# Optimization experiments

Measured on AMD Instinct MI355X. Metric: run time of the kernel, lower is better.

Reference implementation:

```python
import jax, jax.numpy as jnp
import numpy as np

# NSA hyperparams (match init_kwargs)
D_BLK = 64    # d: block stride
L_CMP = 64    # compression block length (== d -> non-overlapping blocks)
L_SLC = 64    # selection block length (== l_cmp == d -> P_slc = P_cmp)
BQ = 64       # block_size_q
TOPK = 16     # slc_top_k
WL, WR = 512, 0  # sliding window (left, right)


def _nsa_forward(q, k, v, w_k, b_k, w_v, b_v, w_gate, b_gate, seqlen):
    S, qh, dim = q.shape
    kv = k.shape[1]
    H = qh // kv
    b = S // seqlen          # number of equal-length packed sequences
    s = seqlen
    scale = dim ** -0.5
    f32 = jnp.float32

    # [b, s, kv, H, e]: q head g*H+h belongs to kv head g (repeat_interleave layout)
    q5 = q.reshape(b, s, kv, H, dim)
    k3 = k.reshape(b, s, kv, dim)
    v3 = v.reshape(b, s, kv, dim)

    # ---- block compression (extract_blocks + cmp_linear over block length) ----
    n_blk = s // D_BLK
    kb = k.reshape(b, n_blk, D_BLK, kv, dim)
    vb = v.reshape(b, n_blk, D_BLK, kv, dim)
    K_cmp = jnp.einsum('bntke,t->bnke', kb, w_k) + b_k[0]
    V_cmp = jnp.einsum('bntke,t->bnke', vb, w_v) + b_v[0]

    # ---- compressed attention (per sequence, fp32 softmax) ----
    sc = jnp.einsum('bqkhe,bnke->bkhqn', q5, K_cmp).astype(f32) * scale
    P = jax.nn.softmax(sc, axis=-1)
    out_cmp = jnp.einsum('bkhqn,bnke->bqkhe', P.astype(q.dtype), V_cmp)

    # ---- selection scores: pool P over q-blocks and GQA groups, then top-k ----
    nqb = s // BQ
    pooled = P.reshape(b, kv, H, nqb, BQ, n_blk).sum(axis=(2, 4))  # [b,kv,nqb,n_blk]
    idx = jax.lax.top_k(pooled, TOPK)[1]                            # [b,kv,nqb,TOPK]

    # gather selected K/V blocks (shared by all queries in a q-block / GQA group)
    kb2 = jnp.transpose(kb, (0, 3, 1, 2, 4))  # [b,kv,n_blk,l,e]
    vb2 = jnp.transpose(vb, (0, 3, 1, 2, 4))
    gather = jax.vmap(jax.vmap(lambda blocks, i: blocks[i]))
    K_sel = gather(kb2, idx)  # [b,kv,nqb,TOPK,l,e]
    V_sel = gather(vb2, idx)

    # ---- selected-block attention ----
    qblk = q5.reshape(b, nqb, BQ, kv, H, dim)
    sc2 = jnp.einsum('bnckhe,bkntle->bkhnctl', qblk, K_sel).astype(f32) * scale
    sc2 = sc2.reshape(b, kv, H, nqb, BQ, TOPK * L_SLC)
    P2 = jax.nn.softmax(sc2, axis=-1).astype(q.dtype)
    out_slc = jnp.einsum('bkhncm,bknme->bnckhe', P2,
                         V_sel.reshape(b, kv, nqb, TOPK * L_SLC, dim))
    out_slc = out_slc.reshape(b, s, kv, H, dim)

    # ---- sliding-window attention (window_size=(WL, WR), non-causal flag) ----
    sw = jnp.einsum('bikhe,bjke->bkhij', q5, k3).astype(f32) * scale
    i = jnp.arange(s)[:, None]
    j = jnp.arange(s)[None, :]
    valid = (j >= i - WL) & (j <= i + WR)
    sw = jnp.where(valid, sw, -jnp.inf)
    Pw = jax.nn.softmax(sw, axis=-1).astype(q.dtype)
    out_win = jnp.einsum('bkhij,bjke->bikhe', Pw, v3)

    # ---- gated fusion of the three branches ----
    gate = jax.nn.sigmoid(jnp.einsum('bqkhe,ec->bqkhc', q5, w_gate) + b_gate)
    out = (gate[..., 0:1] * out_cmp
           + gate[..., 1:2] * out_slc
           + gate[..., 2:3] * out_win)
    return out.reshape(S, qh, dim)


def setup_inputs() -> dict:
    key = jax.random.key(0)
    ks = jax.random.split(key, 9)
    S, qh, kvh, dim = 4096, 8, 2, 128
    inp = {
        'q': jax.random.normal(ks[0], (S, qh, dim), jnp.float32),
        'k': jax.random.normal(ks[1], (S, kvh, dim), jnp.float32),
        'v': jax.random.normal(ks[2], (S, kvh, dim), jnp.float32),
        'w_k': jax.random.normal(ks[3], (L_CMP,), jnp.float32) * (L_CMP ** -0.5),
        'b_k': jax.random.normal(ks[4], (1,), jnp.float32) * 0.02,
        'w_v': jax.random.normal(ks[5], (L_CMP,), jnp.float32) * (L_CMP ** -0.5),
        'b_v': jax.random.normal(ks[6], (1,), jnp.float32) * 0.02,
        'w_gate': jax.random.normal(ks[7], (dim, 3), jnp.float32) * (dim ** -0.5),
        'b_gate': jax.random.normal(ks[8], (3,), jnp.float32) * 0.02,
        'seqlen': 2048,
    }
    return inp


def reference(q, k, v, w_k, b_k, w_v, b_v, w_gate, b_gate, seqlen):
    return _nsa_forward(q, k, v, w_k, b_k, w_v, b_v, w_gate, b_gate, seqlen)
```

## Files before the change

kernel.cpp:

```cpp
#include <hip/hip_runtime.h>
#include <hip/hip_bf16.h>


#define SEQ   2048
#define NB    2
#define KV    2
#define NH    4
#define QH    8
#define DIM   128
#define NBLK  32
#define NQB   32
#define NTOP  16
#define SCALE 0.08838834764831845f
#define QSC   0.12751831795244785f
#define VP    72
#define VCS   40

typedef unsigned short ushort_t;
using bf16x8 = __attribute__((ext_vector_type(8))) short;
using f32x4  = __attribute__((ext_vector_type(4))) float;

__device__ __forceinline__ unsigned pkbf(float a, float b){
  union { __hip_bfloat162 h; unsigned u; } cv;
  cv.h = __float22bfloat162_rn(make_float2(a, b));
  return cv.u;
}
__device__ __forceinline__ ushort_t b16(float f){
  union { float f; unsigned i; } x; x.f = f;
  unsigned r = x.i + 0x7fffu + ((x.i >> 16) & 1u);
  return (ushort_t)(r >> 16);
}
__device__ __forceinline__ float fb(ushort_t h){
  union { unsigned i; float f; } x; x.i = ((unsigned)h) << 16;
  return x.f;
}

__device__ __forceinline__ void async16(ushort_t* l, const ushort_t* g){
  __builtin_amdgcn_global_load_lds(
      (const __attribute__((address_space(1))) unsigned int*)(size_t)g,
      (__attribute__((address_space(3))) unsigned int*)(size_t)l,
      16, 0, 0);
}

__global__ __launch_bounds__(256) void prep_k(
    const float* __restrict__ k, const float* __restrict__ v,
    const float* __restrict__ w_k, const float* __restrict__ b_k,
    const float* __restrict__ w_v, const float* __restrict__ b_v,
    ushort_t* __restrict__ Kb, ushort_t* __restrict__ VT,
    float* __restrict__ Kc, float* __restrict__ Vc)
{
  int blk = blockIdx.x;
  int db = blk & 1, rb = (blk >> 1) & 31, bbg = blk >> 6;
  int bb = bbg >> 1, g = bbg & 1;
  int tid = threadIdx.x;
  __shared__ ushort_t T[64*VP];
  __shared__ float wks[64], wvs[64];
  __shared__ float accK[16][64], accV[16][64];

  if (tid < 64){ wks[tid] = w_k[tid]; wvs[tid] = w_v[tid]; }
  __syncthreads();

  float4 sk = {0,0,0,0}, sv = {0,0,0,0};
  for (int jj = 0; jj < 4; ++jj){
    int i = tid + jj*256;
    int r = i >> 4, ds = i & 15;
    size_t src = ((size_t)(bb*SEQ + rb*64 + r)*KV + g)*DIM + db*64 + ds*4;
    float4 kx = *(const float4*)(k + src);
    float4 vx = *(const float4*)(v + src);
    uint2 kk; kk.x = pkbf(kx.x,kx.y); kk.y = pkbf(kx.z,kx.w);
    size_t rowb = ((size_t)bbg*SEQ + rb*64 + r)*DIM*2;
    int swz = (db*128 + ds*8) ^ ((r & 7) << 4);
    *(uint2*)((char*)Kb + rowb + swz) = kk;
    unsigned v01 = pkbf(vx.x,vx.y), v23 = pkbf(vx.z,vx.w);
    T[(ds*4+0)*VP + r] = (ushort_t)(v01 & 0xffffu);
    T[(ds*4+1)*VP + r] = (ushort_t)(v01 >> 16);
    T[(ds*4+2)*VP + r] = (ushort_t)(v23 & 0xffffu);
    T[(ds*4+3)*VP + r] = (ushort_t)(v23 >> 16);
    float a = wks[r], b = wvs[r];
    sk.x += a*kx.x; sk.y += a*kx.y; sk.z += a*kx.z; sk.w += a*kx.w;
    sv.x += b*vx.x; sv.y += b*vx.y; sv.z += b*vx.z; sv.w += b*vx.w;
  }
  *(float4*)&accK[tid>>4][(tid&15)*4] = sk;
  *(float4*)&accV[tid>>4][(tid&15)*4] = sv;
  __syncthreads();

  for (int jj = 0; jj < 4; ++jj){
    int i = tid + jj*256;
    int d = i >> 4, seg = i & 15;
    uint2 u = *(uint2*)&T[d*VP + seg*4];
    size_t rowb = ((size_t)bbg*DIM + db*64 + d)*SEQ*2;
    int swz = (seg*8) ^ ((d & 7) << 4);
    *(uint2*)((char*)VT + rowb + rb*128 + swz) = u;
  }

  size_t obase = ((size_t)(bbg*NBLK + rb))*DIM + db*64;
  if (tid < 64){
    float s = 0.f;
#pragma unroll
    for (int i = 0; i < 16; ++i) s += accK[i][tid];
    Kc[obase + tid] = s + b_k[0];
  } else if (tid < 128){
    int d = tid - 64;
    float s = 0.f;
#pragma unroll
    for (int i = 0; i < 16; ++i) s += accV[i][d];
    Vc[obase + d] = s + b_v[0];
  }
}

__global__ __launch_bounds__(512, 2) void attn_k(
    const float* __restrict__ q, const ushort_t* __restrict__ Kb,
    const ushort_t* __restrict__ VT,
    const float* __restrict__ Kc, const float* __restrict__ Vc,
    const float* __restrict__ w_gate, const float* __restrict__ b_gate,
    float* __restrict__ slcbuf, float* __restrict__ out)
{
  int idx = blockIdx.x;
  int x = idx & 7, low = idx & 1, u = idx >> 3;
  int bbg = x >> 1;
  int j = u*2 + low;
  int role = j >> 5;
  int qb = j & 31;
  int bb = bbg >> 1, g = bbg & 1;

  int tid = threadIdx.x;
  int lane = tid & 63, w = tid >> 6;
  int quad = lane >> 4, l15 = lane & 15;
  int h = w & 3, qh2 = w >> 2;
  int xr = (l15 & 7) << 4;

  __shared__ ushort_t Ks[2][64*128];
  __shared__ ushort_t VTs[2][128*64];
  __shared__ ushort_t Ps[256*VP];
  __shared__ ushort_t VcTh[128*VCS];
  __shared__ ushort_t VcTl[128*VCS];
  __shared__ float pw[8][NBLK];
  __shared__ float gbuf[256];
  __shared__ int   idxs[NTOP];

  if (role == 0){
    {
      int key = tid >> 4, dq = tid & 15;
      const float* kcs = Kc + ((size_t)bbg*NBLK + key)*DIM + dq*8;
      float4 f0 = *(const float4*)kcs, f1 = *(const float4*)(kcs + 4);
      float fe[8] = {f0.x,f0.y,f0.z,f0.w,f1.x,f1.y,f1.z,f1.w};
      union { ushort_t u[8]; uint4 v; } hi, lo;
#pragma unroll
      for (int e = 0; e < 8; ++e){
        ushort_t hh = b16(fe[e]);
        hi.u[e] = hh; lo.u[e] = b16(fe[e] - fb(hh));
      }
      int off = (dq*16) ^ ((key & 7) << 4);
      *(uint4*)((char*)&Ks[0][0] + key*256 + off) = hi.v;
      *(uint4*)((char*)&Ks[0][0] + (key+32)*256 + off) = lo.v;
    }
    {
      int d = tid & 127, kq = tid >> 7;
      const float* vcs = Vc + (size_t)bbg*NBLK*DIM + d;
      union { ushort_t u[8]; uint4 v; } hi, lo;
#pragma unroll
      for (int kk = 0; kk < 8; ++kk){
        float f = vcs[(kq*8 + kk)*DIM];
        ushort_t hh = b16(f);
        hi.u[kk] = hh; lo.u[kk] = b16(f - fb(hh));
      }
      *(uint4*)&VcTh[d*VCS + kq*8] = hi.v;
      *(uint4*)&VcTl[d*VCS + kq*8] = lo.v;
    }
  }

  const float* qrow0 = q + ((size_t)(bb*SEQ + qb*64 + qh2*32 + l15)*QH + g*NH + h)*DIM;
  const float* qrow1 = qrow0 + (size_t)16*QH*DIM;
  int gcol = 1 + role;
  bf16x8 qfrag0[4], qfrag1[4], qlo0[4], qlo1[4];
  float gp0 = 0.f, gp1 = 0.f, gc0 = 0.f, gc1 = 0.f;
#pragma unroll
  for (int kc = 0; kc < 4; ++kc){
    int d0 = kc*32 + quad*8;
    float4 a0 = *(const float4*)(qrow0 + d0);
    float4 a1 = *(const float4*)(qrow0 + d0 + 4);
    float4 b0 = *(const float4*)(qrow1 + d0);
    float4 b1 = *(const float4*)(qrow1 + d0 + 4);
    float qa[8] = {a0.x,a0.y,a0.z,a0.w,a1.x,a1.y,a1.z,a1.w};
    float qc[8] = {b0.x,b0.y,b0.z,b0.w,b1.x,b1.y,b1.z,b1.w};
#pragma unroll
    for (int jj = 0; jj < 8; ++jj){
      float wg = w_gate[(d0+jj)*3 + gcol];
      gp0 += qa[jj]*wg; gp1 += qc[jj]*wg;
    }
    if (role == 0){
#pragma unroll
      for (int jj = 0; jj < 8; ++jj){
        float w0 = w_gate[(d0+jj)*3];
        gc0 += qa[jj]*w0; gc1 += qc[jj]*w0;
      }
      union { ushort_t u[8]; bf16x8 v; } h0, l0, h1, l1;
#pragma unroll
      for (int e = 0; e < 8; ++e){
        float s0f = qa[e]*QSC; ushort_t hh0 = b16(s0f);
        h0.u[e] = hh0; l0.u[e] = b16(s0f - fb(hh0));
        float s1f = qc[e]*QSC; ushort_t hh1 = b16(s1f);
        h1.u[e] = hh1; l1.u[e] = b16(s1f - fb(hh1));
      }
      qfrag0[kc] = h0.v; qlo0[kc] = l0.v;
      qfrag1[kc] = h1.v; qlo1[kc] = l1.v;
    } else {
      union { unsigned uu[4]; bf16x8 v8; } t0, t1;
#pragma unroll
      for (int p2 = 0; p2 < 4; ++p2){
        t0.uu[p2] = pkbf(qa[2*p2]*QSC, qa[2*p2+1]*QSC);
        t1.uu[p2] = pkbf(qc[2*p2]*QSC, qc[2*p2+1]*QSC);
      }
      qfrag0[kc] = t0.v8; qfrag1[kc] = t1.v8;
    }
  }
  gp0 += __shfl_xor(gp0,16); gp0 += __shfl_xor(gp0,32);
  gp1 += __shfl_xor(gp1,16); gp1 += __shfl_xor(gp1,32);
  if (quad == 0){
    gbuf[w*32 + l15]      = 1.f/(1.f + __expf(-(gp0 + b_gate[gcol])));
    gbuf[w*32 + 16 + l15] = 1.f/(1.f + __expf(-(gp1 + b_gate[gcol])));
  }
  float g0c0 = 0.f, g0c1 = 0.f;
  if (role == 0){
    gc0 += __shfl_xor(gc0,16); gc0 += __shfl_xor(gc0,32);
    gc1 += __shfl_xor(gc1,16); gc1 += __shfl_xor(gc1,32);
    g0c0 = 1.f/(1.f + __expf(-(gc0 + b_gate[0])));
    g0c1 = 1.f/(1.f + __expf(-(gc1 + b_gate[0])));
  }
  __syncthreads();
  float gl0[4], gl1[4];
#pragma unroll
  for (int r = 0; r < 4; ++r){
    gl0[r] = gbuf[w*32 + quad*4 + r];
    gl1[r] = gbuf[w*32 + 16 + quad*4 + r];
  }

  const f32x4 zero4 = {0.f,0.f,0.f,0.f};
  f32x4 cp0[2], cp1[2];
  cp0[0] = zero4; cp0[1] = zero4; cp1[0] = zero4; cp1[1] = zero4;

  if (role == 0){
    f32x4 c0[2], c1[2];
    c0[0]=zero4; c0[1]=zero4; c1[0]=zero4; c1[1]=zero4;
#pragma unroll
    for (int kc = 0; kc < 4; ++kc){
#pragma unroll
      for (int nt = 0; nt < 2; ++nt){
        bf16x8 ah = *(bf16x8*)((char*)&Ks[0][0] + (nt*16 + l15)*256
                               + ((kc*64 + quad*16) ^ xr));
        bf16x8 al = *(bf16x8*)((char*)&Ks[0][0] + (nt*16 + l15 + 32)*256
                               + ((kc*64 + quad*16) ^ xr));
        c0[nt] = __builtin_amdgcn_mfma_f32_16x16x32_bf16(ah, qfrag0[kc], c0[nt], 0, 0, 0);
        c0[nt] = __builtin_amdgcn_mfma_f32_16x16x32_bf16(ah, qlo0[kc],   c0[nt], 0, 0, 0);
        c0[nt] = __builtin_amdgcn_mfma_f32_16x16x32_bf16(al, qfrag0[kc], c0[nt], 0, 0, 0);
        c1[nt] = __builtin_amdgcn_mfma_f32_16x16x32_bf16(ah, qfrag1[kc], c1[nt], 0, 0, 0);
        c1[nt] = __builtin_amdgcn_mfma_f32_16x16x32_bf16(ah, qlo1[kc],   c1[nt], 0, 0, 0);
        c1[nt] = __builtin_amdgcn_mfma_f32_16x16x32_bf16(al, qfrag1[kc], c1[nt], 0, 0, 0);
      }
    }
    float mx0 = -INFINITY, mx1 = -INFINITY;
#pragma unroll
    for (int nt = 0; nt < 2; ++nt)
#pragma unroll
      for (int r = 0; r < 4; ++r){
        mx0 = fmaxf(mx0, c0[nt][r]); mx1 = fmaxf(mx1, c1[nt][r]);
      }
    mx0 = fmaxf(mx0, __shfl_xor(mx0,16)); mx0 = fmaxf(mx0, __shfl_xor(mx0,32));
    mx1 = fmaxf(mx1, __shfl_xor(mx1,16)); mx1 = fmaxf(mx1, __shfl_xor(mx1,32));
    float s0 = 0.f, s1 = 0.f;
#pragma unroll
    for (int nt = 0; nt < 2; ++nt)
#pragma unroll
      for (int r = 0; r < 4; ++r){
        float p0v = exp2f(c0[nt][r] - mx0); c0[nt][r] = p0v; s0 += p0v;
        float p1v = exp2f(c1[nt][r] - mx1); c1[nt][r] = p1v; s1 += p1v;
      }
    s0 += __shfl_xor(s0,16); s0 += __shfl_xor(s0,32);
    s1 += __shfl_xor(s1,16); s1 += __shfl_xor(s1,32);
    float ip0 = 1.f/s0, ip1 = 1.f/s1;
    float ig0 = g0c0*ip0, ig1 = g0c1*ip1;
#pragma unroll
    for (int nt = 0; nt < 2; ++nt)
#pragma unroll
      for (int r = 0; r < 4; ++r){
        cp0[nt][r] = c0[nt][r]*ig0;
        cp1[nt][r] = c1[nt][r]*ig1;
        float t = c0[nt][r]*ip0 + c1[nt][r]*ip1;
        t += __shfl_xor(t,1); t += __shfl_xor(t,2);
        t += __shfl_xor(t,4); t += __shfl_xor(t,8);
        if (l15 == 0) pw[w][nt*16 + quad*4 + r] = t;
      }
    __syncthreads();
    if (tid < 64){
      int n = lane;
      float val = -INFINITY;
      if (n < NBLK){
        float sm = 0.f;
#pragma unroll
        for (int w2 = 0; w2 < 8; ++w2) sm += pw[w2][n];
        val = sm;
      }
      for (int t = 0; t < NTOP; ++t){
        float bv = val; int bi = n;
        for (int mm = 1; mm < 32; mm <<= 1){
          float ov = __shfl_xor(bv, mm);
          int   oi = __shfl_xor(bi, mm);
          if (ov > bv || (ov == bv && oi < bi)){ bv = ov; bi = oi; }
        }
        if (lane == 0) idxs[t] = bi;
        if (n == bi) val = -INFINITY;
      }
    }
    __syncthreads();
  }

  const ushort_t* kbase  = Kb + (size_t)bbg*SEQ*DIM;
  const ushort_t* vtbase = VT + (size_t)bbg*DIM*SEQ;

  int kb0 = (qb >= 8) ? (qb - 8) : 0;
  int nph = (role == 0) ? NTOP : (qb - kb0 + 1);
  int qi0 = qh2*32 + l15, qi1 = qi0 + 16;

  float m10 = -INFINITY, l10 = 0.f, m11 = -INFINITY, l11 = 0.f;
  f32x4 oacc0[8], oacc1[8];
#pragma unroll
  for (int dt = 0; dt < 8; ++dt){ oacc0[dt] = zero4; oacc1[dt] = zero4; }

  auto stage = [&](int bufi, int kb_){
    const ushort_t* ksrc = kbase + (size_t)kb_*64*DIM;
#pragma unroll
    for (int jj = 0; jj < 2; ++jj)
      async16(&Ks[bufi][(jj*512 + w*64)*8], ksrc + (size_t)(tid + jj*512)*8);
    const ushort_t* vsrc = vtbase + kb_*64;
#pragma unroll
    for (int jj = 0; jj < 2; ++jj){
      int i = tid + jj*512;
      int d = i >> 3, sg = i & 7;
      async16(&VTs[bufi][(jj*512 + w*64)*8], vsrc + (size_t)d*SEQ + sg*8);
    }
  };

  stage(0, (role == 0) ? idxs[0] : kb0);

  for (int t = 0; t < nph; ++t){
    int cur = t & 1;
    int kb = (role == 0) ? idxs[t] : (kb0 + t);
    __syncthreads();
    if (t+1 < nph){
      int kbn = (role == 0) ? idxs[t+1] : (kb0 + t + 1);
      stage(cur ^ 1, kbn);
    }
    __builtin_amdgcn_sched_barrier(0);

    f32x4 sacc0[4], sacc1[4];
#pragma unroll
    for (int nt = 0; nt < 4; ++nt){ sacc0[nt] = zero4; sacc1[nt] = zero4; }
    __builtin_amdgcn_s_setprio(1);
#pragma unroll
    for (int kc = 0; kc < 4; ++kc){
#pragma unroll
      for (int nt = 0; nt < 4; ++nt){
        bf16x8 a = *(bf16x8*)((char*)&Ks[cur][0] + (nt*16 + l15)*256
                              + ((kc*64 + quad*16) ^ xr));
        sacc0[nt] = __builtin_amdgcn_mfma_f32_16x16x32_bf16(a, qfrag0[kc], sacc0[nt], 0, 0, 0);
        sacc1[nt] = __builtin_amdgcn_mfma_f32_16x16x32_bf16(a, qfrag1[kc], sacc1[nt], 0, 0, 0);
      }
    }
    __builtin_amdgcn_s_setprio(0);

    bool mlow  = (role == 1) && (kb == qb - 8);
    bool mhigh = (role == 1) && (kb == qb);
    bool domask = mlow | mhigh;

    auto softmax_qt = [&](f32x4* sc2, float& m1r, float& l1r, int qi_l,
                          bool& skipped) -> float {
      float mx = -INFINITY;
      if (domask){
#pragma unroll
        for (int nt = 0; nt < 4; ++nt)
#pragma unroll
          for (int r = 0; r < 4; ++r){
            int key = nt*16 + quad*4 + r;
            float sv = sc2[nt][r];
            bool valid = (!mlow || key >= qi_l) && (!mhigh || key <= qi_l);
            sv = valid ? sv : -INFINITY;
            sc2[nt][r] = sv;
            mx = fmaxf(mx, sv);
          }
      } else {
#pragma unroll
        for (int nt = 0; nt < 4; ++nt)
#pragma unroll
          for (int r = 0; r < 4; ++r) mx = fmaxf(mx, sc2[nt][r]);
      }
      mx = fmaxf(mx, __shfl_xor(mx, 16));
      mx = fmaxf(mx, __shfl_xor(mx, 32));
      float al = 1.f;
      skipped = __all(mx <= m1r + 8.f);
      if (!skipped){
        float mn = fmaxf(m1r, mx);
        al = exp2f(m1r - mn);
        m1r = mn;
      }
      float s0 = 0.f;
#pragma unroll
      for (int nt = 0; nt < 4; ++nt)
#pragma unroll
        for (int r = 0; r < 4; ++r){
          float pe = exp2f(sc2[nt][r] - m1r);
          sc2[nt][r] = pe;
          s0 += pe;
        }
      s0 += __shfl_xor(s0, 16);
      s0 += __shfl_xor(s0, 32);
      l1r = l1r*al + s0;
      return al;
    };
    bool sk0, sk1;
    float al0 = softmax_qt(sacc0, m10, l10, qi0, sk0);
    float al1 = softmax_qt(sacc1, m11, l11, qi1, sk1);

#pragma unroll
    for (int nt = 0; nt < 4; ++nt){
      uint2 p0, p1;
      p0.x = pkbf(sacc0[nt][0], sacc0[nt][1]);
      p0.y = pkbf(sacc0[nt][2], sacc0[nt][3]);
      p1.x = pkbf(sacc1[nt][0], sacc1[nt][1]);
      p1.y = pkbf(sacc1[nt][2], sacc1[nt][3]);
      *(uint2*)&Ps[(w*32 + l15)*VP + nt*16 + quad*4] = p0;
      *(uint2*)&Ps[(w*32 + 16 + l15)*VP + nt*16 + quad*4] = p1;
    }

    if (!sk0){
      float ar[4];
#pragma unroll
      for (int r = 0; r < 4; ++r) ar[r] = __shfl(al0, quad*4 + r);
#pragma unroll
      for (int dt = 0; dt < 8; ++dt)
#pragma unroll
        for (int r = 0; r < 4; ++r) oacc0[dt][r] *= ar[r];
    }
    if (!sk1){
      float ar[4];
#pragma unroll
      for (int r = 0; r < 4; ++r) ar[r] = __shfl(al1, quad*4 + r);
#pragma unroll
      for (int dt = 0; dt < 8; ++dt)
#pragma unroll
        for (int r = 0; r < 4; ++r) oacc1[dt][r] *= ar[r];
    }

#pragma unroll
    for (int kc2 = 0; kc2 < 2; ++kc2){
      bf16x8 pa0 = *(bf16x8*)&Ps[(w*32 + l15)*VP + kc2*32 + quad*8];
      bf16x8 pa1 = *(bf16x8*)&Ps[(w*32 + 16 + l15)*VP + kc2*32 + quad*8];
      __builtin_amdgcn_s_setprio(1);
#pragma unroll
      for (int dt = 0; dt < 8; ++dt){
        bf16x8 vb8 = *(bf16x8*)((char*)&VTs[cur][0] + (dt*16 + l15)*128
                                + ((kc2*64 + quad*16) ^ xr));
        oacc0[dt] = __builtin_amdgcn_mfma_f32_16x16x32_bf16(pa0, vb8, oacc0[dt], 0, 0, 0);
        oacc1[dt] = __builtin_amdgcn_mfma_f32_16x16x32_bf16(pa1, vb8, oacc1[dt], 0, 0, 0);
      }
      __builtin_amdgcn_s_setprio(0);
    }
  }

  float lr0[4], lr1[4];
#pragma unroll
  for (int r = 0; r < 4; ++r){
    lr0[r] = __shfl(l10, quad*4 + r);
    lr1[r] = __shfl(l11, quad*4 + r);
  }
  if (role == 0){
    float a0[4], a1[4];
#pragma unroll
    for (int r = 0; r < 4; ++r){ a0[r] = gl0[r]/lr0[r]; a1[r] = gl1[r]/lr1[r]; }
#pragma unroll
    for (int dt = 0; dt < 8; ++dt)
#pragma unroll
      for (int r = 0; r < 4; ++r){ oacc0[dt][r] *= a0[r]; oacc1[dt][r] *= a1[r]; }
#pragma unroll
    for (int nt = 0; nt < 2; ++nt){
      union { ushort_t u[4]; uint2 v; } h0, l0, h1, l1;
#pragma unroll
      for (int r = 0; r < 4; ++r){
        ushort_t hh0 = b16(cp0[nt][r]);
        h0.u[r] = hh0; l0.u[r] = b16(cp0[nt][r] - fb(hh0));
        ushort_t hh1 = b16(cp1[nt][r]);
        h1.u[r] = hh1; l1.u[r] = b16(cp1[nt][r] - fb(hh1));
      }
      *(uint2*)&Ps[(w*32 + l15)*VP + nt*16 + quad*4]      = h0.v;
      *(uint2*)&Ps[(w*32 + l15)*VP + 32 + nt*16 + quad*4] = l0.v;
      *(uint2*)&Ps[(w*32 + 16 + l15)*VP + nt*16 + quad*4]      = h1.v;
      *(uint2*)&Ps[(w*32 + 16 + l15)*VP + 32 + nt*16 + quad*4] = l1.v;
    }
    bf16x8 pah0 = *(bf16x8*)&Ps[(w*32 + l15)*VP + quad*8];
    bf16x8 pal0 = *(bf16x8*)&Ps[(w*32 + l15)*VP + 32 + quad*8];
    bf16x8 pah1 = *(bf16x8*)&Ps[(w*32 + 16 + l15)*VP + quad*8];
    bf16x8 pal1 = *(bf16x8*)&Ps[(w*32 + 16 + l15)*VP + 32 + quad*8];
#pragma unroll
    for (int dt = 0; dt < 8; ++dt){
      bf16x8 vbh = *(bf16x8*)&VcTh[(dt*16 + l15)*VCS + quad*8];
      bf16x8 vbl = *(bf16x8*)&VcTl[(dt*16 + l15)*VCS + quad*8];
      oacc0[dt] = __builtin_amdgcn_mfma_f32_16x16x32_bf16(pah0, vbh, oacc0[dt], 0, 0, 0);
      oacc0[dt] = __builtin_amdgcn_mfma_f32_16x16x32_bf16(pah0, vbl, oacc0[dt], 0, 0, 0);
      oacc0[dt] = __builtin_amdgcn_mfma_f32_16x16x32_bf16(pal0, vbh, oacc0[dt], 0, 0, 0);
      oacc1[dt] = __builtin_amdgcn_mfma_f32_16x16x32_bf16(pah1, vbh, oacc1[dt], 0, 0, 0);
      oacc1[dt] = __builtin_amdgcn_mfma_f32_16x16x32_bf16(pah1, vbl, oacc1[dt], 0, 0, 0);
      oacc1[dt] = __builtin_amdgcn_mfma_f32_16x16x32_bf16(pal1, vbh, oacc1[dt], 0, 0, 0);
    }
#pragma unroll
    for (int r = 0; r < 4; ++r){
      size_t ob0 = ((size_t)(bb*SEQ + qb*64 + qh2*32 + quad*4 + r)*QH + g*NH + h)*DIM + l15;
      size_t ob1 = ob0 + (size_t)16*QH*DIM;
      float* op0 = slcbuf + ob0;
      float* op1 = slcbuf + ob1;
#pragma unroll
      for (int dt = 0; dt < 8; ++dt){
        op0[dt*16] = oacc0[dt][r];
        op1[dt*16] = oacc1[dt][r];
      }
    }
  } else {
#pragma unroll
    for (int r = 0; r < 4; ++r){
      float s20 = gl0[r] / lr0[r];
      float s21 = gl1[r] / lr1[r];
      size_t ob0 = ((size_t)(bb*SEQ + qb*64 + qh2*32 + quad*4 + r)*QH + g*NH + h)*DIM + l15;
      size_t ob1 = ob0 + (size_t)16*QH*DIM;
      float* op0 = out + ob0;
      float* op1 = out + ob1;
#pragma unroll
      for (int dt = 0; dt < 8; ++dt){
        op0[dt*16] = s20 * oacc0[dt][r];
        op1[dt*16] = s21 * oacc1[dt][r];
      }
    }
  }
}

__global__ __launch_bounds__(256) void merge_k(const float* __restrict__ slcbuf,
                                               float* __restrict__ out){
  int i = blockIdx.x * 256 + threadIdx.x;
  float4 a = ((const float4*)slcbuf)[i];
  float4 b = ((float4*)out)[i];
  b.x += a.x; b.y += a.y; b.z += a.z; b.w += a.w;
  ((float4*)out)[i] = b;
}

extern "C" void kernel_launch(void* const* d_in, const int* in_sizes, int n_in,
                              void* d_out, int out_size, void* d_ws, size_t ws_size,
                              hipStream_t stream) {
  const float* q      = (const float*)d_in[0];
  const float* k      = (const float*)d_in[1];
  const float* v      = (const float*)d_in[2];
  const float* w_k    = (const float*)d_in[3];
  const float* b_k    = (const float*)d_in[4];
  const float* w_v    = (const float*)d_in[5];
  const float* b_v    = (const float*)d_in[6];
  const float* w_gate = (const float*)d_in[7];
  const float* b_gate = (const float*)d_in[8];
  float* out = (float*)d_out;

  float* ws     = (float*)d_ws;
  float* Kc     = ws;
  float* Vc     = ws + 16384;
  float* slcbuf = ws + 49152;
  ushort_t* Kb  = (ushort_t*)(ws + 4243456);
  ushort_t* VT  = Kb + 1048576;

  prep_k <<<256, 256, 0, stream>>>(k, v, w_k, b_k, w_v, b_v, Kb, VT, Kc, Vc);
  attn_k <<<256, 512, 0, stream>>>(q, Kb, VT, Kc, Vc, w_gate, b_gate, slcbuf, out);
  merge_k<<<4096, 256, 0, stream>>>(slcbuf, out);
}
```

Measured before the change: 166.3 us.

## Software-pipeline PV matmul one step behind QK and use bitonic top-k

The attention loop now runs the P·V MFMA for the previous key block after the QK MFMA of the current block, so the softmax of one step overlaps with matrix work of another. To support this, V tiles get a third LDS buffer rotated between prev/cur/next, and the final P·V step is drained after the loop. The iterative 16-round shuffle argmax top-k is replaced by one bitonic sort over the 32 pooled scores, and the max and sum reductions are rewritten as trees. The cost is more LDS use and extra live registers for the deferred rescale state, which could reduce occupancy.

```diff
diff --git a/kernel.cpp b/kernel.cpp
--- a/kernel.cpp
+++ b/kernel.cpp
@@ -130,7 +130,7 @@
   int xr = (l15 & 7) << 4;
 
   __shared__ ushort_t Ks[2][64*128];
-  __shared__ ushort_t VTs[2][128*64];
+  __shared__ ushort_t VTs[3][128*64];
   __shared__ ushort_t Ps[256*VP];
   __shared__ ushort_t VcTh[128*VCS];
   __shared__ ushort_t VcTl[128*VCS];
@@ -300,16 +300,19 @@
         for (int w2 = 0; w2 < 8; ++w2) sm += pw[w2][n];
         val = sm;
       }
-      for (int t = 0; t < NTOP; ++t){
-        float bv = val; int bi = n;
-        for (int mm = 1; mm < 32; mm <<= 1){
-          float ov = __shfl_xor(bv, mm);
-          int   oi = __shfl_xor(bi, mm);
-          if (ov > bv || (ov == bv && oi < bi)){ bv = ov; bi = oi; }
+      int idxv = n;
+      for (int kk = 2; kk <= 32; kk <<= 1){
+        for (int jj2 = kk >> 1; jj2 > 0; jj2 >>= 1){
+          float pv = __shfl_xor(val, jj2);
+          int   pi = __shfl_xor(idxv, jj2);
+          bool lower = (lane & jj2) == 0;
+          bool desc  = (lane & kk) == 0;
+          bool iwin  = (val > pv) || (val == pv && idxv < pi);
+          bool keep  = (lower == desc) ? iwin : !iwin;
+          if (!keep){ val = pv; idxv = pi; }
         }
-        if (lane == 0) idxs[t] = bi;
-        if (n == bi) val = -INFINITY;
-      }
+      }
+      if (lane < NTOP) idxs[lane] = idxv;
     }
     __syncthreads();
   }
@@ -326,29 +329,32 @@
 #pragma unroll
   for (int dt = 0; dt < 8; ++dt){ oacc0[dt] = zero4; oacc1[dt] = zero4; }
 
-  auto stage = [&](int bufi, int kb_){
+  auto stage = [&](int kbuf, int vbuf, int kb_){
     const ushort_t* ksrc = kbase + (size_t)kb_*64*DIM;
 #pragma unroll
     for (int jj = 0; jj < 2; ++jj)
-      async16(&Ks[bufi][(jj*512 + w*64)*8], ksrc + (size_t)(tid + jj*512)*8);
+      async16(&Ks[kbuf][(jj*512 + w*64)*8], ksrc + (size_t)(tid + jj*512)*8);
     const ushort_t* vsrc = vtbase + kb_*64;
 #pragma unroll
     for (int jj = 0; jj < 2; ++jj){
       int i = tid + jj*512;
       int d = i >> 3, sg = i & 7;
-      async16(&VTs[bufi][(jj*512 + w*64)*8], vsrc + (size_t)d*SEQ + sg*8);
+      async16(&VTs[vbuf][(jj*512 + w*64)*8], vsrc + (size_t)d*SEQ + sg*8);
     }
   };
 
-  stage(0, (role == 0) ? idxs[0] : kb0);
+  stage(0, 0, (role == 0) ? idxs[0] : kb0);
+
+  float alp0 = 1.f, alp1 = 1.f;
+  bool  skp0 = true,  skp1 = true;
+  int vprev = 2, vcur = 0, vnext = 1;
 
   for (int t = 0; t < nph; ++t){
-    int cur = t & 1;
     int kb = (role == 0) ? idxs[t] : (kb0 + t);
     __syncthreads();
     if (t+1 < nph){
       int kbn = (role == 0) ? idxs[t+1] : (kb0 + t + 1);
-      stage(cur ^ 1, kbn);
+      stage((t+1) & 1, vnext, kbn);
     }
     __builtin_amdgcn_sched_barrier(0);
 
@@ -360,7 +366,7 @@
     for (int kc = 0; kc < 4; ++kc){
 #pragma unroll
       for (int nt = 0; nt < 4; ++nt){
-        bf16x8 a = *(bf16x8*)((char*)&Ks[cur][0] + (nt*16 + l15)*256
+        bf16x8 a = *(bf16x8*)((char*)&Ks[t & 1][0] + (nt*16 + l15)*256
                               + ((kc*64 + quad*16) ^ xr));
         sacc0[nt] = __builtin_amdgcn_mfma_f32_16x16x32_bf16(a, qfrag0[kc], sacc0[nt], 0, 0, 0);
         sacc1[nt] = __builtin_amdgcn_mfma_f32_16x16x32_bf16(a, qfrag1[kc], sacc1[nt], 0, 0, 0);
@@ -368,31 +374,63 @@
     }
     __builtin_amdgcn_s_setprio(0);
 
+    if (t > 0){
+      if (!skp0){
+        float ar[4];
+#pragma unroll
+        for (int r = 0; r < 4; ++r) ar[r] = __shfl(alp0, quad*4 + r);
+#pragma unroll
+        for (int dt = 0; dt < 8; ++dt)
+#pragma unroll
+          for (int r = 0; r < 4; ++r) oacc0[dt][r] *= ar[r];
+      }
+      if (!skp1){
+        float ar[4];
+#pragma unroll
+        for (int r = 0; r < 4; ++r) ar[r] = __shfl(alp1, quad*4 + r);
+#pragma unroll
+        for (int dt = 0; dt < 8; ++dt)
+#pragma unroll
+          for (int r = 0; r < 4; ++r) oacc1[dt][r] *= ar[r];
+      }
+#pragma unroll
+      for (int kc2 = 0; kc2 < 2; ++kc2){
+        bf16x8 pa0 = *(bf16x8*)&Ps[(w*32 + l15)*VP + kc2*32 + quad*8];
+        bf16x8 pa1 = *(bf16x8*)&Ps[(w*32 + 16 + l15)*VP + kc2*32 + quad*8];
+        __builtin_amdgcn_s_setprio(1);
+#pragma unroll
+        for (int dt = 0; dt < 8; ++dt){
+          bf16x8 vb8 = *(bf16x8*)((char*)&VTs[vprev][0] + (dt*16 + l15)*128
+                                  + ((kc2*64 + quad*16) ^ xr));
+          oacc0[dt] = __builtin_amdgcn_mfma_f32_16x16x32_bf16(pa0, vb8, oacc0[dt], 0, 0, 0);
+          oacc1[dt] = __builtin_amdgcn_mfma_f32_16x16x32_bf16(pa1, vb8, oacc1[dt], 0, 0, 0);
+        }
+        __builtin_amdgcn_s_setprio(0);
+      }
+    }
+
     bool mlow  = (role == 1) && (kb == qb - 8);
     bool mhigh = (role == 1) && (kb == qb);
     bool domask = mlow | mhigh;
 
     auto softmax_qt = [&](f32x4* sc2, float& m1r, float& l1r, int qi_l,
                           bool& skipped) -> float {
-      float mx = -INFINITY;
       if (domask){
 #pragma unroll
         for (int nt = 0; nt < 4; ++nt)
 #pragma unroll
           for (int r = 0; r < 4; ++r){
             int key = nt*16 + quad*4 + r;
-            float sv = sc2[nt][r];
             bool valid = (!mlow || key >= qi_l) && (!mhigh || key <= qi_l);
-            sv = valid ? sv : -INFINITY;
-            sc2[nt][r] = sv;
-            mx = fmaxf(mx, sv);
+            sc2[nt][r] = valid ? sc2[nt][r] : -INFINITY;
           }
-      } else {
-#pragma unroll
-        for (int nt = 0; nt < 4; ++nt)
-#pragma unroll
-          for (int r = 0; r < 4; ++r) mx = fmaxf(mx, sc2[nt][r]);
-      }
+      }
+      float mnt[4];
+#pragma unroll
+      for (int nt = 0; nt < 4; ++nt)
+        mnt[nt] = fmaxf(fmaxf(sc2[nt][0], sc2[nt][1]),
+                        fmaxf(sc2[nt][2], sc2[nt][3]));
+      float mx = fmaxf(fmaxf(mnt[0], mnt[1]), fmaxf(mnt[2], mnt[3]));
       mx = fmaxf(mx, __shfl_xor(mx, 16));
       mx = fmaxf(mx, __shfl_xor(mx, 32));
       float al = 1.f;
@@ -402,15 +440,17 @@
         al = exp2f(m1r - mn);
         m1r = mn;
       }
-      float s0 = 0.f;
-#pragma unroll
-      for (int nt = 0; nt < 4; ++nt)
-#pragma unroll
-        for (int r = 0; r < 4; ++r){
-          float pe = exp2f(sc2[nt][r] - m1r);
-          sc2[nt][r] = pe;
-          s0 += pe;
-        }
+      float snt[4];
+#pragma unroll
+      for (int nt = 0; nt < 4; ++nt){
+        float p0 = exp2f(sc2[nt][0] - m1r);
+        float p1 = exp2f(sc2[nt][1] - m1r);
+        float p2 = exp2f(sc2[nt][2] - m1r);
+        float p3 = exp2f(sc2[nt][3] - m1r);
+        sc2[nt][0] = p0; sc2[nt][1] = p1; sc2[nt][2] = p2; sc2[nt][3] = p3;
+        snt[nt] = (p0 + p1) + (p2 + p3);
+      }
+      float s0 = (snt[0] + snt[1]) + (snt[2] + snt[3]);
       s0 += __shfl_xor(s0, 16);
       s0 += __shfl_xor(s0, 32);
       l1r = l1r*al + s0;
@@ -419,6 +459,8 @@
     bool sk0, sk1;
     float al0 = softmax_qt(sacc0, m10, l10, qi0, sk0);
     float al1 = softmax_qt(sacc1, m11, l11, qi1, sk1);
+    alp0 = al0; skp0 = sk0;
+    alp1 = al1; skp1 = sk1;
 
 #pragma unroll
     for (int nt = 0; nt < 4; ++nt){
@@ -431,38 +473,39 @@
       *(uint2*)&Ps[(w*32 + 16 + l15)*VP + nt*16 + quad*4] = p1;
     }
 
-    if (!sk0){
+    int tmpv = vprev; vprev = vcur; vcur = vnext; vnext = tmpv;
+  }
+
+  {
+    if (!skp0){
       float ar[4];
 #pragma unroll
-      for (int r = 0; r < 4; ++r) ar[r] = __shfl(al0, quad*4 + r);
+      for (int r = 0; r < 4; ++r) ar[r] = __shfl(alp0, quad*4 + r);
 #pragma unroll
       for (int dt = 0; dt < 8; ++dt)
 #pragma unroll
         for (int r = 0; r < 4; ++r) oacc0[dt][r] *= ar[r];
     }
-    if (!sk1){
+    if (!skp1){
       float ar[4];
 #pragma unroll
-      for (int r = 0; r < 4; ++r) ar[r] = __shfl(al1, quad*4 + r);
+      for (int r = 0; r < 4; ++r) ar[r] = __shfl(alp1, quad*4 + r);
 #pragma unroll
       for (int dt = 0; dt < 8; ++dt)
 #pragma unroll
         for (int r = 0; r < 4; ++r) oacc1[dt][r] *= ar[r];
     }
-
 #pragma unroll
     for (int kc2 = 0; kc2 < 2; ++kc2){
       bf16x8 pa0 = *(bf16x8*)&Ps[(w*32 + l15)*VP + kc2*32 + quad*8];
       bf16x8 pa1 = *(bf16x8*)&Ps[(w*32 + 16 + l15)*VP + kc2*32 + quad*8];
-      __builtin_amdgcn_s_setprio(1);
 #pragma unroll
       for (int dt = 0; dt < 8; ++dt){
-        bf16x8 vb8 = *(bf16x8*)((char*)&VTs[cur][0] + (dt*16 + l15)*128
+        bf16x8 vb8 = *(bf16x8*)((char*)&VTs[vprev][0] + (dt*16 + l15)*128
                                 + ((kc2*64 + quad*16) ^ xr));
         oacc0[dt] = __builtin_amdgcn_mfma_f32_16x16x32_bf16(pa0, vb8, oacc0[dt], 0, 0, 0);
         oacc1[dt] = __builtin_amdgcn_mfma_f32_16x16x32_bf16(pa1, vb8, oacc1[dt], 0, 0, 0);
       }
-      __builtin_amdgcn_s_setprio(0);
     }
   }
 
```

After: 162.9 us, median of 2. 2.1% less time.

## Process two KV blocks per iteration, read V from global, bitonic top-k

Applied to the files above, without the earlier changes.

Each attention iteration now handles two 64-key blocks (128 keys), which halves the number of phases and barriers. K is double-buffered in shared memory, while V^T is read directly from global memory into MFMA operands instead of being staged, and the V^T swizzle is dropped. The serial 16-round top-k arg-max is replaced with a wavefront bitonic sort. In exchange, register pressure rises from wider score tiles, V loads become unstaged global reads with possible latency stalls, and the window path adds an extra masked half-block.

```diff
diff --git a/kernel.cpp b/kernel.cpp
--- a/kernel.cpp
+++ b/kernel.cpp
@@ -14,6 +14,7 @@
 #define SCALE 0.08838834764831845f
 #define QSC   0.12751831795244785f
 #define VP    72
+#define PSP   136
 #define VCS   40
 
 typedef unsigned short ushort_t;
@@ -89,8 +90,7 @@
     int d = i >> 4, seg = i & 15;
     uint2 u = *(uint2*)&T[d*VP + seg*4];
     size_t rowb = ((size_t)bbg*DIM + db*64 + d)*SEQ*2;
-    int swz = (seg*8) ^ ((d & 7) << 4);
-    *(uint2*)((char*)VT + rowb + rb*128 + swz) = u;
+    *(uint2*)((char*)VT + rowb + rb*128 + seg*8) = u;
   }
 
   size_t obase = ((size_t)(bbg*NBLK + rb))*DIM + db*64;
@@ -129,9 +129,8 @@
   int h = w & 3, qh2 = w >> 2;
   int xr = (l15 & 7) << 4;
 
-  __shared__ ushort_t Ks[2][64*128];
-  __shared__ ushort_t VTs[2][128*64];
-  __shared__ ushort_t Ps[256*VP];
+  __shared__ ushort_t Ks[2][128*128];
+  __shared__ ushort_t Ps[256*PSP];
   __shared__ ushort_t VcTh[128*VCS];
   __shared__ ushort_t VcTl[128*VCS];
   __shared__ float pw[8][NBLK];
@@ -300,16 +299,19 @@
         for (int w2 = 0; w2 < 8; ++w2) sm += pw[w2][n];
         val = sm;
       }
-      for (int t = 0; t < NTOP; ++t){
-        float bv = val; int bi = n;
-        for (int mm = 1; mm < 32; mm <<= 1){
-          float ov = __shfl_xor(bv, mm);
-          int   oi = __shfl_xor(bi, mm);
-          if (ov > bv || (ov == bv && oi < bi)){ bv = ov; bi = oi; }
+      int idxv = n;
+      for (int kk = 2; kk <= 32; kk <<= 1){
+        for (int jj2 = kk >> 1; jj2 > 0; jj2 >>= 1){
+          float pv = __shfl_xor(val, jj2);
+          int   pi = __shfl_xor(idxv, jj2);
+          bool lower = (lane & jj2) == 0;
+          bool desc  = (lane & kk) == 0;
+          bool iwin  = (val > pv) || (val == pv && idxv < pi);
+          bool keep  = (lower == desc) ? iwin : !iwin;
+          if (!keep){ val = pv; idxv = pi; }
         }
-        if (lane == 0) idxs[t] = bi;
-        if (n == bi) val = -INFINITY;
-      }
+      }
+      if (lane < NTOP) idxs[lane] = idxv;
     }
     __syncthreads();
   }
@@ -318,48 +320,50 @@
   const ushort_t* vtbase = VT + (size_t)bbg*DIM*SEQ;
 
   int kb0 = (qb >= 8) ? (qb - 8) : 0;
-  int nph = (role == 0) ? NTOP : (qb - kb0 + 1);
+  int nph = (role == 0) ? 8 : ((qb < 8) ? ((qb >> 1) + 1) : 5);
   int qi0 = qh2*32 + l15, qi1 = qi0 + 16;
+  int hc0 = qb*64 + qi0 - kb0*64 - (nph - 1)*128;
+  int hc1 = hc0 + 16;
 
   float m10 = -INFINITY, l10 = 0.f, m11 = -INFINITY, l11 = 0.f;
   f32x4 oacc0[8], oacc1[8];
 #pragma unroll
   for (int dt = 0; dt < 8; ++dt){ oacc0[dt] = zero4; oacc1[dt] = zero4; }
 
-  auto stage = [&](int bufi, int kb_){
-    const ushort_t* ksrc = kbase + (size_t)kb_*64*DIM;
-#pragma unroll
-    for (int jj = 0; jj < 2; ++jj)
-      async16(&Ks[bufi][(jj*512 + w*64)*8], ksrc + (size_t)(tid + jj*512)*8);
-    const ushort_t* vsrc = vtbase + kb_*64;
-#pragma unroll
-    for (int jj = 0; jj < 2; ++jj){
-      int i = tid + jj*512;
-      int d = i >> 3, sg = i & 7;
-      async16(&VTs[bufi][(jj*512 + w*64)*8], vsrc + (size_t)d*SEQ + sg*8);
+  auto stageK = [&](int bufi, int rA, int rB){
+#pragma unroll
+    for (int jj = 0; jj < 4; ++jj){
+      int unit = tid + jj*512;
+      int row = unit >> 4, seg = unit & 15;
+      int absrow = (row < 64) ? (rA + row) : (rB + row - 64);
+      async16(&Ks[bufi][(jj*512 + w*64)*8],
+              kbase + (size_t)absrow*DIM + seg*8);
     }
   };
 
-  stage(0, (role == 0) ? idxs[0] : kb0);
+  if (role == 0) stageK(0, idxs[0]*64, idxs[1]*64);
+  else           stageK(0, kb0*64, kb0*64 + 64);
 
   for (int t = 0; t < nph; ++t){
     int cur = t & 1;
-    int kb = (role == 0) ? idxs[t] : (kb0 + t);
     __syncthreads();
     if (t+1 < nph){
-      int kbn = (role == 0) ? idxs[t+1] : (kb0 + t + 1);
-      stage(cur ^ 1, kbn);
+      if (role == 0) stageK(cur ^ 1, idxs[2*t+2]*64, idxs[2*t+3]*64);
+      else {
+        int rA = kb0*64 + (t+1)*128;
+        stageK(cur ^ 1, rA, rA + 64);
+      }
     }
     __builtin_amdgcn_sched_barrier(0);
 
-    f32x4 sacc0[4], sacc1[4];
-#pragma unroll
-    for (int nt = 0; nt < 4; ++nt){ sacc0[nt] = zero4; sacc1[nt] = zero4; }
+    f32x4 sacc0[8], sacc1[8];
+#pragma unroll
+    for (int nt = 0; nt < 8; ++nt){ sacc0[nt] = zero4; sacc1[nt] = zero4; }
     __builtin_amdgcn_s_setprio(1);
 #pragma unroll
     for (int kc = 0; kc < 4; ++kc){
 #pragma unroll
-      for (int nt = 0; nt < 4; ++nt){
+      for (int nt = 0; nt < 8; ++nt){
         bf16x8 a = *(bf16x8*)((char*)&Ks[cur][0] + (nt*16 + l15)*256
                               + ((kc*64 + quad*16) ^ xr));
         sacc0[nt] = __builtin_amdgcn_mfma_f32_16x16x32_bf16(a, qfrag0[kc], sacc0[nt], 0, 0, 0);
@@ -368,31 +372,29 @@
     }
     __builtin_amdgcn_s_setprio(0);
 
-    bool mlow  = (role == 1) && (kb == qb - 8);
-    bool mhigh = (role == 1) && (kb == qb);
-    bool domask = mlow | mhigh;
+    bool mlowP  = (role == 1) && (qb >= 8) && (t == 0);
+    bool mhighP = (role == 1) && (t == nph - 1);
+    bool domask = mlowP | mhighP;
 
     auto softmax_qt = [&](f32x4* sc2, float& m1r, float& l1r, int qi_l,
-                          bool& skipped) -> float {
-      float mx = -INFINITY;
+                          int hc_l, bool& skipped) -> float {
       if (domask){
 #pragma unroll
-        for (int nt = 0; nt < 4; ++nt)
+        for (int nt = 0; nt < 8; ++nt)
 #pragma unroll
           for (int r = 0; r < 4; ++r){
-            int key = nt*16 + quad*4 + r;
-            float sv = sc2[nt][r];
-            bool valid = (!mlow || key >= qi_l) && (!mhigh || key <= qi_l);
-            sv = valid ? sv : -INFINITY;
-            sc2[nt][r] = sv;
-            mx = fmaxf(mx, sv);
+            int kl = nt*16 + quad*4 + r;
+            bool valid = (!mlowP || kl >= qi_l) && (!mhighP || kl <= hc_l);
+            sc2[nt][r] = valid ? sc2[nt][r] : -INFINITY;
           }
-      } else {
-#pragma unroll
-        for (int nt = 0; nt < 4; ++nt)
-#pragma unroll
-          for (int r = 0; r < 4; ++r) mx = fmaxf(mx, sc2[nt][r]);
-      }
+      }
+      float mnt[8];
+#pragma unroll
+      for (int nt = 0; nt < 8; ++nt)
+        mnt[nt] = fmaxf(fmaxf(sc2[nt][0], sc2[nt][1]),
+                        fmaxf(sc2[nt][2], sc2[nt][3]));
+      float mx = fmaxf(fmaxf(fmaxf(mnt[0], mnt[1]), fmaxf(mnt[2], mnt[3])),
+                       fmaxf(fmaxf(mnt[4], mnt[5]), fmaxf(mnt[6], mnt[7])));
       mx = fmaxf(mx, __shfl_xor(mx, 16));
       mx = fmaxf(mx, __shfl_xor(mx, 32));
       float al = 1.f;
@@ -402,33 +404,36 @@
         al = exp2f(m1r - mn);
         m1r = mn;
       }
-      float s0 = 0.f;
-#pragma unroll
-      for (int nt = 0; nt < 4; ++nt)
-#pragma unroll
-        for (int r = 0; r < 4; ++r){
-          float pe = exp2f(sc2[nt][r] - m1r);
-          sc2[nt][r] = pe;
-          s0 += pe;
-        }
+      float snt[8];
+#pragma unroll
+      for (int nt = 0; nt < 8; ++nt){
+        float p0 = exp2f(sc2[nt][0] - m1r);
+        float p1 = exp2f(sc2[nt][1] - m1r);
+        float p2 = exp2f(sc2[nt][2] - m1r);
+        float p3 = exp2f(sc2[nt][3] - m1r);
+        sc2[nt][0] = p0; sc2[nt][1] = p1; sc2[nt][2] = p2; sc2[nt][3] = p3;
+        snt[nt] = (p0 + p1) + (p2 + p3);
+      }
+      float s0 = ((snt[0] + snt[1]) + (snt[2] + snt[3]))
+               + ((snt[4] + snt[5]) + (snt[6] + snt[7]));
       s0 += __shfl_xor(s0, 16);
       s0 += __shfl_xor(s0, 32);
       l1r = l1r*al + s0;
       return al;
     };
     bool sk0, sk1;
-    float al0 = softmax_qt(sacc0, m10, l10, qi0, sk0);
-    float al1 = softmax_qt(sacc1, m11, l11, qi1, sk1);
-
-#pragma unroll
-    for (int nt = 0; nt < 4; ++nt){
+    float al0 = softmax_qt(sacc0, m10, l10, qi0, hc0, sk0);
+    float al1 = softmax_qt(sacc1, m11, l11, qi1, hc1, sk1);
+
+#pragma unroll
+    for (int nt = 0; nt < 8; ++nt){
       uint2 p0, p1;
       p0.x = pkbf(sacc0[nt][0], sacc0[nt][1]);
       p0.y = pkbf(sacc0[nt][2], sacc0[nt][3]);
       p1.x = pkbf(sacc1[nt][0], sacc1[nt][1]);
       p1.y = pkbf(sacc1[nt][2], sacc1[nt][3]);
-      *(uint2*)&Ps[(w*32 + l15)*VP + nt*16 + quad*4] = p0;
-      *(uint2*)&Ps[(w*32 + 16 + l15)*VP + nt*16 + quad*4] = p1;
+      *(uint2*)&Ps[(w*32 + l15)*PSP + nt*16 + quad*4] = p0;
+      *(uint2*)&Ps[(w*32 + 16 + l15)*PSP + nt*16 + quad*4] = p1;
     }
 
     if (!sk0){
@@ -451,16 +456,22 @@
     }
 
 #pragma unroll
-    for (int kc2 = 0; kc2 < 2; ++kc2){
-      bf16x8 pa0 = *(bf16x8*)&Ps[(w*32 + l15)*VP + kc2*32 + quad*8];
-      bf16x8 pa1 = *(bf16x8*)&Ps[(w*32 + 16 + l15)*VP + kc2*32 + quad*8];
+    for (int kc2 = 0; kc2 < 4; ++kc2){
+      int kg;
+      if (role == 0) kg = idxs[2*t + (kc2 >> 1)]*64 + (kc2 & 1)*32 + quad*8;
+      else {
+        kg = kb0*64 + t*128 + kc2*32 + quad*8;
+        kg = (kg < SEQ) ? kg : 0;
+      }
+      bf16x8 pa0 = *(bf16x8*)&Ps[(w*32 + l15)*PSP + kc2*32 + quad*8];
+      bf16x8 pa1 = *(bf16x8*)&Ps[(w*32 + 16 + l15)*PSP + kc2*32 + quad*8];
+      const ushort_t* vp = vtbase + (size_t)l15*SEQ + kg;
       __builtin_amdgcn_s_setprio(1);
 #pragma unroll
       for (int dt = 0; dt < 8; ++dt){
-        bf16x8 vb8 = *(bf16x8*)((char*)&VTs[cur][0] + (dt*16 + l15)*128
-                                + ((kc2*64 + quad*16) ^ xr));
-        oacc0[dt] = __builtin_amdgcn_mfma_f32_16x16x32_bf16(pa0, vb8, oacc0[dt], 0, 0, 0);
-        oacc1[dt] = __builtin_amdgcn_mfma_f32_16x16x32_bf16(pa1, vb8, oacc1[dt], 0, 0, 0);
+        bf16x8 vb = *(bf16x8*)(vp + (size_t)dt*16*SEQ);
+        oacc0[dt] = __builtin_amdgcn_mfma_f32_16x16x32_bf16(pa0, vb, oacc0[dt], 0, 0, 0);
+        oacc1[dt] = __builtin_amdgcn_mfma_f32_16x16x32_bf16(pa1, vb, oacc1[dt], 0, 0, 0);
       }
       __builtin_amdgcn_s_setprio(0);
     }
@@ -490,15 +501,15 @@
         ushort_t hh1 = b16(cp1[nt][r]);
         h1.u[r] = hh1; l1.u[r] = b16(cp1[nt][r] - fb(hh1));
       }
-      *(uint2*)&Ps[(w*32 + l15)*VP + nt*16 + quad*4]      = h0.v;
-      *(uint2*)&Ps[(w*32 + l15)*VP + 32 + nt*16 + quad*4] = l0.v;
-      *(uint2*)&Ps[(w*32 + 16 + l15)*VP + nt*16 + quad*4]      = h1.v;
-      *(uint2*)&Ps[(w*32 + 16 + l15)*VP + 32 + nt*16 + quad*4] = l1.v;
-    }
-    bf16x8 pah0 = *(bf16x8*)&Ps[(w*32 + l15)*VP + quad*8];
-    bf16x8 pal0 = *(bf16x8*)&Ps[(w*32 + l15)*VP + 32 + quad*8];
-    bf16x8 pah1 = *(bf16x8*)&Ps[(w*32 + 16 + l15)*VP + quad*8];
-    bf16x8 pal1 = *(bf16x8*)&Ps[(w*32 + 16 + l15)*VP + 32 + quad*8];
+      *(uint2*)&Ps[(w*32 + l15)*PSP + nt*16 + quad*4]      = h0.v;
+      *(uint2*)&Ps[(w*32 + l15)*PSP + 32 + nt*16 + quad*4] = l0.v;
+      *(uint2*)&Ps[(w*32 + 16 + l15)*PSP + nt*16 + quad*4]      = h1.v;
+      *(uint2*)&Ps[(w*32 + 16 + l15)*PSP + 32 + nt*16 + quad*4] = l1.v;
+    }
+    bf16x8 pah0 = *(bf16x8*)&Ps[(w*32 + l15)*PSP + quad*8];
+    bf16x8 pal0 = *(bf16x8*)&Ps[(w*32 + l15)*PSP + 32 + quad*8];
+    bf16x8 pah1 = *(bf16x8*)&Ps[(w*32 + 16 + l15)*PSP + quad*8];
+    bf16x8 pal1 = *(bf16x8*)&Ps[(w*32 + 16 + l15)*PSP + 32 + quad*8];
 #pragma unroll
     for (int dt = 0; dt < 8; ++dt){
       bf16x8 vbh = *(bf16x8*)&VcTh[(dt*16 + l15)*VCS + quad*8];
```

After: 199.8 us. 20.1% more time.
